# Optimization experiments

Hardware: AMD Instinct MI355X
Metric: run time of the kernel (lower is better)

Reference implementation:

```python
import jax, jax.numpy as jnp
import numpy as np

N_INPUTS = 128
N_LATENT = 21
LEN_TIME = 51
NUM_SHIFTS = 50
BATCH = 2048
N_HIDDEN = 4  # hidden relu layers in the outer DenseResBlock


def setup_inputs() -> dict:
    key = jax.random.key(0)
    ks = jax.random.split(key, 8)
    s = 0.05  # small init scale keeps activations sane through the residual stack
    return {
        "inputs": jax.random.normal(ks[0], (BATCH, LEN_TIME, N_INPUTS), jnp.float32),
        "L": jnp.eye(N_LATENT, dtype=jnp.float32)
             + s * jax.random.normal(ks[1], (N_LATENT, N_LATENT), jnp.float32),
        "ienc_W": s * jax.random.normal(ks[2], (N_INPUTS, N_LATENT), jnp.float32),
        "idec_W": s * jax.random.normal(ks[3], (N_LATENT, N_INPUTS), jnp.float32),
        "enc_W": s * jax.random.normal(ks[4], (N_HIDDEN, N_INPUTS, N_INPUTS), jnp.float32),
        "enc_b": jnp.zeros((N_HIDDEN, N_INPUTS), jnp.float32),
        "enc_Wo": s * jax.random.normal(ks[5], (N_INPUTS, N_INPUTS), jnp.float32),
        "enc_bo": jnp.zeros((N_INPUTS,), jnp.float32),
        "dec_W": s * jax.random.normal(ks[6], (N_HIDDEN, N_INPUTS, N_INPUTS), jnp.float32),
        "dec_b": jnp.zeros((N_HIDDEN, N_INPUTS), jnp.float32),
        "dec_Wo": s * jax.random.normal(ks[7], (N_INPUTS, N_INPUTS), jnp.float32),
        "dec_bo": jnp.zeros((N_INPUTS,), jnp.float32),
    }


def _resblock(x, W, b, Wo, bo):
    # DenseResBlock: stack of relu Dense layers + linear output + residual skip.
    h = x
    for i in range(W.shape[0]):  # fixed small layer count
        h = jax.nn.relu(h @ W[i] + b[i])
    return x + h @ Wo + bo


def reference(inputs, L, ienc_W, idec_W, enc_W, enc_b, enc_Wo, enc_bo,
              dec_W, dec_b, dec_Wo, dec_bo):
    B, T, n_in = inputs.shape
    len_pred = T - NUM_SHIFTS  # = 1

    auto_in = inputs.reshape(-1, n_in)                        # [B*T, n_in]
    pred_in = inputs[:, :len_pred, :].reshape(-1, n_in)       # [B*len_pred, n_in]

    # autoencoder path
    pe = _resblock(auto_in, enc_W, enc_b, enc_Wo, enc_bo)     # partially encoded
    fe = pe @ ienc_W                                          # fully encoded [., n_latent]
    pd = fe @ idec_W                                          # partially decoded
    autoencoder_output = _resblock(pd, dec_W, dec_b, dec_Wo, dec_bo)
    outer_auto_output = _resblock(pe, dec_W, dec_b, dec_Wo, dec_bo)

    # latent rollout: z_{k+1} = z_k @ L, decode every step
    pe_pred = _resblock(pred_in, enc_W, enc_b, enc_Wo, enc_bo)
    z0 = pe_pred @ ienc_W                                     # [B*len_pred, n_latent]

    def step(z, _):
        z_next = z @ L
        return z_next, z_next

    _, zs = jax.lax.scan(step, z0, None, length=NUM_SHIFTS)   # [S, B*len_pred, n_latent]

    # decode all shifts in one large batched pass (same math as per-shift decode)
    dec_in = zs.reshape(-1, zs.shape[-1]) @ idec_W            # [S*B*len_pred, n_in]
    dec_all = _resblock(dec_in, dec_W, dec_b, dec_Wo, dec_bo)
    predictions = (dec_all
                   .reshape(NUM_SHIFTS, B, len_pred, n_in)
                   .transpose(1, 0, 2, 3)
                   .reshape(B, NUM_SHIFTS * len_pred, n_in))

    return autoencoder_output, outer_auto_output, predictions
```

## Files before the change

### kernel.cpp

```cpp
#include <hip/hip_runtime.h>

#define NF 128
#define NLAT 21
#define NBATCH 2048
#define LEN_T 51
#define NSHIFT 50
#define AUTO_ROWS (NBATCH*LEN_T)
#define PRED_ROWS (NBATCH*NSHIFT)

typedef short bh8  __attribute__((ext_vector_type(8)));
typedef unsigned short us8 __attribute__((ext_vector_type(8)));
typedef float f32x4  __attribute__((ext_vector_type(4)));
typedef float f32x16 __attribute__((ext_vector_type(16)));
typedef unsigned u32x4 __attribute__((ext_vector_type(4)));

#define MFMA32(A,B,C) __builtin_amdgcn_mfma_f32_32x32x16_bf16(A,B,C,0,0,0)
#define SGB(m,n) __builtin_amdgcn_sched_group_barrier((m),(n),0)

__device__ __forceinline__ float bf2f(short s){
  unsigned u = ((unsigned)(unsigned short)s) << 16;
  return __builtin_bit_cast(float, u);
}
__device__ __forceinline__ short f2bf(float v){
  unsigned u = __builtin_bit_cast(unsigned, v);
  return (short)((u + 0x7FFFu + ((u>>16)&1u)) >> 16);
}
__device__ __forceinline__ unsigned pk2(float a, float b){
  unsigned ua = __builtin_bit_cast(unsigned, a) + 0x8000u;
  unsigned ub = __builtin_bit_cast(unsigned, b) + 0x8000u;
  return (ua >> 16) | (ub & 0xFFFF0000u);
}

__global__ void k_mmul(const float* __restrict__ ienc, const float* __restrict__ idec,
                       float* __restrict__ M){
  int idx = blockIdx.x*256 + threadIdx.x;
  int i = idx>>7, j = idx&127;
  float s = 0.f;
#pragma unroll
  for(int k=0;k<NLAT;++k) s = fmaf(ienc[i*NLAT+k], idec[k*NF+j], s);
  M[idx] = s;
}

__global__ void k_prep(const float* __restrict__ encW, const float* __restrict__ encWo,
                       const float* __restrict__ decW, const float* __restrict__ decWo,
                       const float* __restrict__ M,    const float* __restrict__ idec,
                       unsigned short* __restrict__ swz){
  int id  = blockIdx.x*256 + threadIdx.x;
  int mat = id >> 11;
  int rem = id & 2047;
  int f   = rem >> 6, l = rem & 63;
  int s   = f >> 2,  mt = f & 3;
  int hl  = l >> 5,  c  = l & 31;
  const float* src;
  if(mat<4)       src = encW + mat*16384;
  else if(mat==4) src = encWo;
  else if(mat<9)  src = decW + (mat-5)*16384;
  else if(mat==9) src = decWo;
  else if(mat==10)src = M;
  else            src = idec;
  us8 w8;
#pragma unroll
  for(int i=0;i<8;++i){
    int k = s*16 + 4*hl + (i&3) + 8*(i>>2);
    float v;
    if(mat==11) v = (k<NLAT) ? src[k*NF + mt*32 + c] : 0.f;
    else        v = src[k*NF + mt*32 + c];
    w8[i] = (unsigned short)f2bf(v);
  }
  *(us8*)(swz + (size_t)mat*16384 + (size_t)f*512 + (size_t)l*8) = w8;
}

__device__ __forceinline__ bh8 ldg8(const unsigned short* p){ return *(const bh8*)p; }

__device__ __forceinline__ void run_half(const unsigned short* __restrict__ wg, int m,
    const bh8 h[16], f32x16 acc[4], int lane){
  f32x16 z;
#pragma unroll
  for(int r=0;r<16;++r) z[r]=0.f;
  acc[0]=z; acc[1]=z; acc[2]=z; acc[3]=z;
  const unsigned short* base = wg + m*1024 + lane*8;
  bh8 w0a = ldg8(base);
  bh8 w0b = ldg8(base + 512);
  bh8 w1a = ldg8(base + 2048);
  bh8 w1b = ldg8(base + 2048 + 512);
#pragma unroll
  for(int s=0;s<8;++s){
    bh8 na, nb;
    if(s<6){
      na = ldg8(base + (s+2)*2048);
      nb = ldg8(base + (s+2)*2048 + 512);
      SGB(0x20,2);
    }
    __builtin_amdgcn_s_setprio(1);
    acc[0]=MFMA32(w0a,h[s],  acc[0]);
    acc[1]=MFMA32(w0b,h[s],  acc[1]);
    acc[2]=MFMA32(w0a,h[8+s],acc[2]);
    acc[3]=MFMA32(w0b,h[8+s],acc[3]);
    __builtin_amdgcn_s_setprio(0);
    SGB(0x8,4);
    if(s<6){ w0a=w1a; w0b=w1b; w1a=na; w1b=nb; }
    else    { w0a=w1a; w0b=w1b; }
  }
}

__device__ __forceinline__ void run_half_k2(const unsigned short* __restrict__ wg, int m,
    const bh8 zf[4], f32x16 acc[4], int lane){
  f32x16 z;
#pragma unroll
  for(int r=0;r<16;++r) z[r]=0.f;
  acc[0]=z; acc[1]=z; acc[2]=z; acc[3]=z;
  const unsigned short* base = wg + m*1024 + lane*8;
#pragma unroll
  for(int s=0;s<2;++s){
    bh8 a0 = ldg8(base + s*2048);
    bh8 a1 = ldg8(base + s*2048 + 512);
    acc[0]=MFMA32(a0,zf[s],  acc[0]);
    acc[1]=MFMA32(a1,zf[s],  acc[1]);
    acc[2]=MFMA32(a0,zf[2+s],acc[2]);
    acc[3]=MFMA32(a1,zf[2+s],acc[3]);
  }
}

__device__ __forceinline__ void epi_hidden_half(const f32x16 acc[4], const float* __restrict__ bl,
    int m, int hl, bh8 out[8]){
#pragma unroll
  for(int t=0;t<2;++t){
    f32x4 b[4];
#pragma unroll
    for(int q=0;q<4;++q) b[q] = *(const f32x4*)(bl + (2*m+t)*32 + q*8 + hl*4);
#pragma unroll
    for(int g=0;g<2;++g){
      f32x16 a = acc[g*2+t];
#pragma unroll
      for(int q=0;q<4;++q)
#pragma unroll
        for(int j=0;j<4;++j) a[q*4+j] = fmaxf(a[q*4+j] + b[q][j], 0.f);
#pragma unroll
      for(int p=0;p<2;++p){
        u32x4 w;
#pragma unroll
        for(int j=0;j<4;++j) w[j] = pk2(a[p*8+2*j], a[p*8+2*j+1]);
        out[g*4+t*2+p] = __builtin_bit_cast(bh8, w);
      }
    }
  }
}
__device__ __forceinline__ void epi_plain_half(const f32x16 acc[4], bh8 out[8]){
#pragma unroll
  for(int t=0;t<2;++t)
#pragma unroll
    for(int g=0;g<2;++g){
      f32x16 a = acc[g*2+t];
#pragma unroll
      for(int p=0;p<2;++p){
        u32x4 w;
#pragma unroll
        for(int j=0;j<4;++j) w[j] = pk2(a[p*8+2*j], a[p*8+2*j+1]);
        out[g*4+t*2+p] = __builtin_bit_cast(bh8, w);
      }
    }
}

__device__ __forceinline__ void final_half(float* outp, size_t ro0, size_t ro1,
    const f32x16 acc[4], const float* __restrict__ bo, const bh8 r8[8], int m, int hl){
#pragma unroll
  for(int t=0;t<2;++t){
    f32x4 b[4];
#pragma unroll
    for(int q=0;q<4;++q) b[q]=*(const f32x4*)(bo + (2*m+t)*32 + q*8 + hl*4);
#pragma unroll
    for(int g=0;g<2;++g){
      f32x16 a = acc[g*2+t];
      bh8 r0 = r8[g*4 + t*2], r1 = r8[g*4 + t*2 + 1];
#pragma unroll
      for(int q=0;q<4;++q)
#pragma unroll
        for(int j=0;j<4;++j){
          int r=q*4+j;
          a[r] += b[q][j] + bf2f((r<8 ? r0 : r1)[r&7]);
        }
      size_t ro = g ? ro1 : ro0;
#pragma unroll
      for(int q=0;q<4;++q){
        f32x4 w; w[0]=a[q*4+0]; w[1]=a[q*4+1]; w[2]=a[q*4+2]; w[3]=a[q*4+3];
        *(f32x4*)(outp + ro + (2*m+t)*32 + q*8 + hl*4) = w;
      }
    }
  }
}

__device__ __forceinline__ void peWo_half(const f32x16 acc[4], const float* __restrict__ bo,
    const bh8 r8[8], int m, int hl, bh8 out[8], float* __restrict__ pe0,
    int bidx0, int bidx1, bool isz0, bool isz1){
#pragma unroll
  for(int t=0;t<2;++t){
    f32x4 b[4];
#pragma unroll
    for(int q=0;q<4;++q) b[q]=*(const f32x4*)(bo + (2*m+t)*32 + q*8 + hl*4);
#pragma unroll
    for(int g=0;g<2;++g){
      f32x16 a = acc[g*2+t];
      bh8 r0 = r8[g*4 + t*2], r1 = r8[g*4 + t*2 + 1];
#pragma unroll
      for(int q=0;q<4;++q)
#pragma unroll
        for(int j=0;j<4;++j){
          int r=q*4+j;
          a[r] += b[q][j] + bf2f((r<8 ? r0 : r1)[r&7]);
        }
      bool isz = g ? isz1 : isz0;
      int bidx = g ? bidx1 : bidx0;
      if(isz){
#pragma unroll
        for(int q=0;q<4;++q){
          f32x4 w; w[0]=a[q*4+0]; w[1]=a[q*4+1]; w[2]=a[q*4+2]; w[3]=a[q*4+3];
          *(f32x4*)(pe0 + (size_t)bidx*NF + (2*m+t)*32 + q*8 + hl*4) = w;
        }
      }
#pragma unroll
      for(int p=0;p<2;++p){
        u32x4 w;
#pragma unroll
        for(int j=0;j<4;++j) w[j]=pk2(a[p*8+2*j], a[p*8+2*j+1]);
        out[g*4+t*2+p]=__builtin_bit_cast(bh8,w);
      }
    }
  }
}

__device__ __forceinline__ void layer_hidden(const unsigned short* __restrict__ wg,
    const float* __restrict__ bl, bh8 h[16], int lane, int hl){
  f32x16 acc[4]; bh8 t0[8], t1[8];
  run_half(wg,0,h,acc,lane);
  epi_hidden_half(acc,bl,0,hl,t0);
  run_half(wg,1,h,acc,lane);
  epi_hidden_half(acc,bl,1,hl,t1);
#pragma unroll
  for(int g=0;g<2;++g)
#pragma unroll
    for(int k=0;k<4;++k){ h[g*8+k]=t0[g*4+k]; h[g*8+4+k]=t1[g*4+k]; }
}

__device__ __forceinline__ void stash16(unsigned short* sp, const bh8 h[16], int lane){
#pragma unroll
  for(int f=0;f<16;++f) *(bh8*)(sp + f*512 + lane*8) = h[f];
}
__device__ __forceinline__ void unstash16(const unsigned short* sp, bh8 r[16], int lane){
#pragma unroll
  for(int f=0;f<16;++f) r[f] = *(const bh8*)(sp + f*512 + lane*8);
}
__device__ __forceinline__ void unstash8(const unsigned short* sp, bh8 r8[8], int m, int lane){
#pragma unroll
  for(int g=0;g<2;++g)
#pragma unroll
    for(int k=0;k<4;++k)
      r8[g*4+k] = *(const bh8*)(sp + (g*8 + 4*m + k)*512 + lane*8);
}

__global__ __launch_bounds__(64,2)
void k_main4(const float* __restrict__ gin, const unsigned short* __restrict__ swz,
             const float* __restrict__ encB, const float* __restrict__ encBo,
             const float* __restrict__ decB, const float* __restrict__ decBo,
             float* __restrict__ out1, float* __restrict__ out2, float* __restrict__ pe0){
  __shared__ __align__(16) unsigned short sres[8192];
  const int lane = threadIdx.x;
  const int hl = lane>>5, c31 = lane&31;
  const size_t rowbase = (size_t)blockIdx.x*64;
  const int row0 = (int)rowbase + c31, row1 = row0 + 32;
  const size_t ro0 = (size_t)row0*NF, ro1 = (size_t)row1*NF;
  const int bidx0 = row0/LEN_T, bidx1 = row1/LEN_T;
  const bool isz0 = (row0 == bidx0*LEN_T), isz1 = (row1 == bidx1*LEN_T);
  bh8 h[16];

#pragma unroll
  for(int g=0;g<2;++g){
    const float* rp = gin + (g?ro1:ro0);
#pragma unroll
    for(int s=0;s<8;++s){
      f32x4 a=*(const f32x4*)(rp + s*16 + 4*hl);
      f32x4 b=*(const f32x4*)(rp + s*16 + 8 + 4*hl);
      us8 o;
#pragma unroll
      for(int i=0;i<4;++i){ o[i]=(unsigned short)f2bf(a[i]); o[i+4]=(unsigned short)f2bf(b[i]); }
      h[g*8+s]=__builtin_bit_cast(bh8,o);
    }
  }
  stash16(sres, h, lane);

#pragma unroll 1
  for(int l=0;l<4;++l)
    layer_hidden(swz + (size_t)l*16384, encB + l*NF, h, lane, hl);

  {
    const unsigned short* wg = swz + (size_t)4*16384;
    f32x16 acc[4]; bh8 t0[8], t1[8], r8[8];
    run_half(wg,0,h,acc,lane);
    unstash8(sres, r8, 0, lane);
    peWo_half(acc, encBo, r8, 0, hl, t0, pe0, bidx0,bidx1, isz0,isz1);
    run_half(wg,1,h,acc,lane);
    unstash8(sres, r8, 1, lane);
    peWo_half(acc, encBo, r8, 1, hl, t1, pe0, bidx0,bidx1, isz0,isz1);
#pragma unroll
    for(int g=0;g<2;++g)
#pragma unroll
      for(int k=0;k<4;++k){ h[g*8+k]=t0[g*4+k]; h[g*8+4+k]=t1[g*4+k]; }
    stash16(sres, h, lane);
  }

#pragma unroll 1
  for(int l=0;l<4;++l)
    layer_hidden(swz + (size_t)(5+l)*16384, decB + l*NF, h, lane, hl);

  {
    const unsigned short* wg = swz + (size_t)9*16384;
    f32x16 acc[4]; bh8 r8[8];
    run_half(wg,0,h,acc,lane);
    unstash8(sres, r8, 0, lane);
    final_half(out2, ro0, ro1, acc, decBo, r8, 0, hl);
    run_half(wg,1,h,acc,lane);
    unstash8(sres, r8, 1, lane);
    final_half(out2, ro0, ro1, acc, decBo, r8, 1, hl);
  }

  {
    unstash16(sres, h, lane);
    const unsigned short* wg = swz + (size_t)10*16384;
    f32x16 acc[4]; bh8 t0[8], t1[8];
    run_half(wg,0,h,acc,lane); epi_plain_half(acc,t0);
    run_half(wg,1,h,acc,lane); epi_plain_half(acc,t1);
#pragma unroll
    for(int g=0;g<2;++g)
#pragma unroll
      for(int k=0;k<4;++k){ h[g*8+k]=t0[g*4+k]; h[g*8+4+k]=t1[g*4+k]; }
    stash16(sres, h, lane);
  }

#pragma unroll 1
  for(int l=0;l<4;++l)
    layer_hidden(swz + (size_t)(5+l)*16384, decB + l*NF, h, lane, hl);

  {
    const unsigned short* wg = swz + (size_t)9*16384;
    f32x16 acc[4]; bh8 r8[8];
    run_half(wg,0,h,acc,lane);
    unstash8(sres, r8, 0, lane);
    final_half(out1, ro0, ro1, acc, decBo, r8, 0, hl);
    run_half(wg,1,h,acc,lane);
    unstash8(sres, r8, 1, lane);
    final_half(out1, ro0, ro1, acc, decBo, r8, 1, hl);
  }
}

__global__ void k_roll(const float* __restrict__ pe0, const float* __restrict__ ienc,
                       const float* __restrict__ L, float* __restrict__ zs){
  const int tid=threadIdx.x, lane=tid&63, wid=tid>>6, sub=lane&31, half=lane>>5;
  const int row=blockIdx.x*8 + wid*2 + half;
  const bool act = sub < NLAT;
  float Lc[NLAT];
#pragma unroll
  for(int k=0;k<NLAT;++k) Lc[k] = act ? L[k*NLAT+sub] : 0.f;
  float z=0.f;
  if(act){
    const float* pr = pe0 + (size_t)row*NF;
    float s0=0.f,s1=0.f,s2=0.f,s3=0.f;
#pragma unroll 8
    for(int k=0;k<NF;k+=4){
      s0=fmaf(pr[k+0], ienc[(k+0)*NLAT+sub], s0);
      s1=fmaf(pr[k+1], ienc[(k+1)*NLAT+sub], s1);
      s2=fmaf(pr[k+2], ienc[(k+2)*NLAT+sub], s2);
      s3=fmaf(pr[k+3], ienc[(k+3)*NLAT+sub], s3);
    }
    z=(s0+s1)+(s2+s3);
  }
  const int base = half*32;
#pragma unroll 1
  for(int s=0;s<NSHIFT;++s){
    float zn=0.f;
#pragma unroll
    for(int k=0;k<NLAT;++k) zn=fmaf(__shfl(z, base+k, 64), Lc[k], zn);
    z=zn;
    if(act) zs[((size_t)s*NBATCH + row)*NLAT + sub] = z;
  }
}

__global__ __launch_bounds__(64,2)
void k_pred4(const float* __restrict__ zs, const unsigned short* __restrict__ swz,
             const float* __restrict__ decB, const float* __restrict__ decBo,
             float* __restrict__ out3){
  __shared__ __align__(16) unsigned short sres[8192];
  const int lane = threadIdx.x;
  const int hl = lane>>5, c31 = lane&31;
  const size_t rowbase = (size_t)blockIdx.x*64;
  const int prow0 = (int)rowbase + c31, prow1 = prow0 + 32;
  const int orow0 = (prow0 & 2047)*NSHIFT + (prow0 >> 11);
  const int orow1 = (prow1 & 2047)*NSHIFT + (prow1 >> 11);
  bh8 h[16];

  bh8 zf[4];
#pragma unroll
  for(int g=0;g<2;++g){
    const float* zr = zs + (size_t)(g?prow1:prow0)*NLAT;
#pragma unroll
    for(int s=0;s<2;++s){
      us8 o;
#pragma unroll
      for(int i=0;i<8;++i){
        int cc = s*16 + 4*hl + (i&3) + 8*(i>>2);
        o[i] = (cc<NLAT) ? (unsigned short)f2bf(zr[cc]) : (unsigned short)0;
      }
      zf[g*2+s]=__builtin_bit_cast(bh8,o);
    }
  }

  {
    const unsigned short* wg = swz + (size_t)11*16384;
    f32x16 acc[4]; bh8 t0[8], t1[8];
    run_half_k2(wg,0,zf,acc,lane); epi_plain_half(acc,t0);
    run_half_k2(wg,1,zf,acc,lane); epi_plain_half(acc,t1);
#pragma unroll
    for(int g=0;g<2;++g)
#pragma unroll
      for(int k=0;k<4;++k){ h[g*8+k]=t0[g*4+k]; h[g*8+4+k]=t1[g*4+k]; }
    stash16(sres, h, lane);
  }

#pragma unroll 1
  for(int l=0;l<4;++l)
    layer_hidden(swz + (size_t)(5+l)*16384, decB + l*NF, h, lane, hl);

  {
    const unsigned short* wg = swz + (size_t)9*16384;
    f32x16 acc[4]; bh8 r8[8];
    run_half(wg,0,h,acc,lane);
    unstash8(sres, r8, 0, lane);
    final_half(out3, (size_t)orow0*NF, (size_t)orow1*NF, acc, decBo, r8, 0, hl);
    run_half(wg,1,h,acc,lane);
    unstash8(sres, r8, 1, lane);
    final_half(out3, (size_t)orow0*NF, (size_t)orow1*NF, acc, decBo, r8, 1, hl);
  }
}

extern "C" void kernel_launch(void* const* d_in, const int* in_sizes, int n_in,
                              void* d_out, int out_size, void* d_ws, size_t ws_size,
                              hipStream_t stream) {
  const float* gin   = (const float*)d_in[0];
  const float* L     = (const float*)d_in[1];
  const float* iencW = (const float*)d_in[2];
  const float* idecW = (const float*)d_in[3];
  const float* encW  = (const float*)d_in[4];
  const float* encB  = (const float*)d_in[5];
  const float* encWo = (const float*)d_in[6];
  const float* encBo = (const float*)d_in[7];
  const float* decW  = (const float*)d_in[8];
  const float* decB  = (const float*)d_in[9];
  const float* decWo = (const float*)d_in[10];
  const float* decBo = (const float*)d_in[11];

  float* out1 = (float*)d_out;
  float* out2 = out1 + (size_t)AUTO_ROWS*NF;
  float* out3 = out2 + (size_t)AUTO_ROWS*NF;

  float* M   = (float*)d_ws;
  float* pe0 = M + 16384;
  float* zs  = pe0 + (size_t)NBATCH*NF;
  unsigned short* swz = (unsigned short*)(zs + (size_t)NSHIFT*NBATCH*NLAT);

  hipLaunchKernelGGL(k_mmul, dim3(64),  dim3(256), 0, stream, iencW, idecW, M);
  hipLaunchKernelGGL(k_prep, dim3(96),  dim3(256), 0, stream, encW, encWo, decW, decWo, M, idecW, swz);
  hipLaunchKernelGGL(k_main4, dim3(AUTO_ROWS/64), dim3(64), 0, stream,
                     gin, swz, encB, encBo, decB, decBo, out1, out2, pe0);
  hipLaunchKernelGGL(k_roll, dim3(NBATCH/8), dim3(256), 0, stream, pe0, iencW, L, zs);
  hipLaunchKernelGGL(k_pred4, dim3(PRED_ROWS/64), dim3(64), 0, stream,
                     zs, swz, decB, decBo, out3);
}
```

Measured before the change: 153.2 us.

## Halve rows per wave to cut registers and raise occupancy

Each 64-lane block now processes 32 rows instead of 64. Accumulators, activation fragments and the shared-memory residual stash are halved, and launch bounds rise from 2 to 3 waves per SIMD. Grids for the main and prediction kernels double to match. The aim is more waves in flight to hide weight-load and MFMA latency. The cost is that each weight fragment loaded from global memory or cache feeds half as many MFMAs, so weight traffic per row doubles.

```diff
diff --git a/kernel.cpp b/kernel.cpp
--- a/kernel.cpp
+++ b/kernel.cpp
@@ -73,11 +73,11 @@
 __device__ __forceinline__ bh8 ldg8(const unsigned short* p){ return *(const bh8*)p; }
 
 __device__ __forceinline__ void run_half(const unsigned short* __restrict__ wg, int m,
-    const bh8 h[16], f32x16 acc[4], int lane){
+    const bh8 h[8], f32x16 acc[2], int lane){
   f32x16 z;
 #pragma unroll
   for(int r=0;r<16;++r) z[r]=0.f;
-  acc[0]=z; acc[1]=z; acc[2]=z; acc[3]=z;
+  acc[0]=z; acc[1]=z;
   const unsigned short* base = wg + m*1024 + lane*8;
   bh8 w0a = ldg8(base);
   bh8 w0b = ldg8(base + 512);
@@ -92,189 +92,164 @@
       SGB(0x20,2);
     }
     __builtin_amdgcn_s_setprio(1);
-    acc[0]=MFMA32(w0a,h[s],  acc[0]);
-    acc[1]=MFMA32(w0b,h[s],  acc[1]);
-    acc[2]=MFMA32(w0a,h[8+s],acc[2]);
-    acc[3]=MFMA32(w0b,h[8+s],acc[3]);
+    acc[0]=MFMA32(w0a,h[s],acc[0]);
+    acc[1]=MFMA32(w0b,h[s],acc[1]);
     __builtin_amdgcn_s_setprio(0);
-    SGB(0x8,4);
+    SGB(0x8,2);
     if(s<6){ w0a=w1a; w0b=w1b; w1a=na; w1b=nb; }
     else    { w0a=w1a; w0b=w1b; }
   }
 }
 
 __device__ __forceinline__ void run_half_k2(const unsigned short* __restrict__ wg, int m,
-    const bh8 zf[4], f32x16 acc[4], int lane){
+    const bh8 zf[2], f32x16 acc[2], int lane){
   f32x16 z;
 #pragma unroll
   for(int r=0;r<16;++r) z[r]=0.f;
-  acc[0]=z; acc[1]=z; acc[2]=z; acc[3]=z;
+  acc[0]=z; acc[1]=z;
   const unsigned short* base = wg + m*1024 + lane*8;
 #pragma unroll
   for(int s=0;s<2;++s){
     bh8 a0 = ldg8(base + s*2048);
     bh8 a1 = ldg8(base + s*2048 + 512);
-    acc[0]=MFMA32(a0,zf[s],  acc[0]);
-    acc[1]=MFMA32(a1,zf[s],  acc[1]);
-    acc[2]=MFMA32(a0,zf[2+s],acc[2]);
-    acc[3]=MFMA32(a1,zf[2+s],acc[3]);
-  }
-}
-
-__device__ __forceinline__ void epi_hidden_half(const f32x16 acc[4], const float* __restrict__ bl,
-    int m, int hl, bh8 out[8]){
+    acc[0]=MFMA32(a0,zf[s],acc[0]);
+    acc[1]=MFMA32(a1,zf[s],acc[1]);
+  }
+}
+
+__device__ __forceinline__ void epi_hidden_half(const f32x16 acc[2], const float* __restrict__ bl,
+    int m, int hl, bh8 out[4]){
 #pragma unroll
   for(int t=0;t<2;++t){
     f32x4 b[4];
 #pragma unroll
     for(int q=0;q<4;++q) b[q] = *(const f32x4*)(bl + (2*m+t)*32 + q*8 + hl*4);
-#pragma unroll
-    for(int g=0;g<2;++g){
-      f32x16 a = acc[g*2+t];
-#pragma unroll
-      for(int q=0;q<4;++q)
-#pragma unroll
-        for(int j=0;j<4;++j) a[q*4+j] = fmaxf(a[q*4+j] + b[q][j], 0.f);
-#pragma unroll
-      for(int p=0;p<2;++p){
-        u32x4 w;
-#pragma unroll
-        for(int j=0;j<4;++j) w[j] = pk2(a[p*8+2*j], a[p*8+2*j+1]);
-        out[g*4+t*2+p] = __builtin_bit_cast(bh8, w);
-      }
-    }
-  }
-}
-__device__ __forceinline__ void epi_plain_half(const f32x16 acc[4], bh8 out[8]){
-#pragma unroll
-  for(int t=0;t<2;++t)
-#pragma unroll
-    for(int g=0;g<2;++g){
-      f32x16 a = acc[g*2+t];
-#pragma unroll
-      for(int p=0;p<2;++p){
-        u32x4 w;
-#pragma unroll
-        for(int j=0;j<4;++j) w[j] = pk2(a[p*8+2*j], a[p*8+2*j+1]);
-        out[g*4+t*2+p] = __builtin_bit_cast(bh8, w);
-      }
-    }
-}
-
-__device__ __forceinline__ void final_half(float* outp, size_t ro0, size_t ro1,
-    const f32x16 acc[4], const float* __restrict__ bo, const bh8 r8[8], int m, int hl){
+    f32x16 a = acc[t];
+#pragma unroll
+    for(int q=0;q<4;++q)
+#pragma unroll
+      for(int j=0;j<4;++j) a[q*4+j] = fmaxf(a[q*4+j] + b[q][j], 0.f);
+#pragma unroll
+    for(int p=0;p<2;++p){
+      u32x4 w;
+#pragma unroll
+      for(int j=0;j<4;++j) w[j] = pk2(a[p*8+2*j], a[p*8+2*j+1]);
+      out[t*2+p] = __builtin_bit_cast(bh8, w);
+    }
+  }
+}
+__device__ __forceinline__ void epi_plain_half(const f32x16 acc[2], bh8 out[4]){
+#pragma unroll
+  for(int t=0;t<2;++t){
+    f32x16 a = acc[t];
+#pragma unroll
+    for(int p=0;p<2;++p){
+      u32x4 w;
+#pragma unroll
+      for(int j=0;j<4;++j) w[j] = pk2(a[p*8+2*j], a[p*8+2*j+1]);
+      out[t*2+p] = __builtin_bit_cast(bh8, w);
+    }
+  }
+}
+
+__device__ __forceinline__ void final_half(float* outp, size_t ro,
+    const f32x16 acc[2], const float* __restrict__ bo, const bh8 r4[4], int m, int hl){
 #pragma unroll
   for(int t=0;t<2;++t){
     f32x4 b[4];
 #pragma unroll
     for(int q=0;q<4;++q) b[q]=*(const f32x4*)(bo + (2*m+t)*32 + q*8 + hl*4);
-#pragma unroll
-    for(int g=0;g<2;++g){
-      f32x16 a = acc[g*2+t];
-      bh8 r0 = r8[g*4 + t*2], r1 = r8[g*4 + t*2 + 1];
-#pragma unroll
-      for(int q=0;q<4;++q)
-#pragma unroll
-        for(int j=0;j<4;++j){
-          int r=q*4+j;
-          a[r] += b[q][j] + bf2f((r<8 ? r0 : r1)[r&7]);
-        }
-      size_t ro = g ? ro1 : ro0;
+    f32x16 a = acc[t];
+    bh8 r0 = r4[t*2], r1 = r4[t*2+1];
+#pragma unroll
+    for(int q=0;q<4;++q)
+#pragma unroll
+      for(int j=0;j<4;++j){
+        int r=q*4+j;
+        a[r] += b[q][j] + bf2f((r<8 ? r0 : r1)[r&7]);
+      }
+#pragma unroll
+    for(int q=0;q<4;++q){
+      f32x4 w; w[0]=a[q*4+0]; w[1]=a[q*4+1]; w[2]=a[q*4+2]; w[3]=a[q*4+3];
+      *(f32x4*)(outp + ro + (2*m+t)*32 + q*8 + hl*4) = w;
+    }
+  }
+}
+
+__device__ __forceinline__ void peWo_half(const f32x16 acc[2], const float* __restrict__ bo,
+    const bh8 r4[4], int m, int hl, bh8 out[4], float* __restrict__ pe0,
+    int bidx, bool isz){
+#pragma unroll
+  for(int t=0;t<2;++t){
+    f32x4 b[4];
+#pragma unroll
+    for(int q=0;q<4;++q) b[q]=*(const f32x4*)(bo + (2*m+t)*32 + q*8 + hl*4);
+    f32x16 a = acc[t];
+    bh8 r0 = r4[t*2], r1 = r4[t*2+1];
+#pragma unroll
+    for(int q=0;q<4;++q)
+#pragma unroll
+      for(int j=0;j<4;++j){
+        int r=q*4+j;
+        a[r] += b[q][j] + bf2f((r<8 ? r0 : r1)[r&7]);
+      }
+    if(isz){
 #pragma unroll
       for(int q=0;q<4;++q){
         f32x4 w; w[0]=a[q*4+0]; w[1]=a[q*4+1]; w[2]=a[q*4+2]; w[3]=a[q*4+3];
-        *(f32x4*)(outp + ro + (2*m+t)*32 + q*8 + hl*4) = w;
+        *(f32x4*)(pe0 + (size_t)bidx*NF + (2*m+t)*32 + q*8 + hl*4) = w;
       }
     }
-  }
-}
-
-__device__ __forceinline__ void peWo_half(const f32x16 acc[4], const float* __restrict__ bo,
-    const bh8 r8[8], int m, int hl, bh8 out[8], float* __restrict__ pe0,
-    int bidx0, int bidx1, bool isz0, bool isz1){
-#pragma unroll
-  for(int t=0;t<2;++t){
-    f32x4 b[4];
-#pragma unroll
-    for(int q=0;q<4;++q) b[q]=*(const f32x4*)(bo + (2*m+t)*32 + q*8 + hl*4);
-#pragma unroll
-    for(int g=0;g<2;++g){
-      f32x16 a = acc[g*2+t];
-      bh8 r0 = r8[g*4 + t*2], r1 = r8[g*4 + t*2 + 1];
-#pragma unroll
-      for(int q=0;q<4;++q)
-#pragma unroll
-        for(int j=0;j<4;++j){
-          int r=q*4+j;
-          a[r] += b[q][j] + bf2f((r<8 ? r0 : r1)[r&7]);
-        }
-      bool isz = g ? isz1 : isz0;
-      int bidx = g ? bidx1 : bidx0;
-      if(isz){
-#pragma unroll
-        for(int q=0;q<4;++q){
-          f32x4 w; w[0]=a[q*4+0]; w[1]=a[q*4+1]; w[2]=a[q*4+2]; w[3]=a[q*4+3];
-          *(f32x4*)(pe0 + (size_t)bidx*NF + (2*m+t)*32 + q*8 + hl*4) = w;
-        }
-      }
-#pragma unroll
-      for(int p=0;p<2;++p){
-        u32x4 w;
-#pragma unroll
-        for(int j=0;j<4;++j) w[j]=pk2(a[p*8+2*j], a[p*8+2*j+1]);
-        out[g*4+t*2+p]=__builtin_bit_cast(bh8,w);
-      }
+#pragma unroll
+    for(int p=0;p<2;++p){
+      u32x4 w;
+#pragma unroll
+      for(int j=0;j<4;++j) w[j]=pk2(a[p*8+2*j], a[p*8+2*j+1]);
+      out[t*2+p]=__builtin_bit_cast(bh8,w);
     }
   }
 }
 
 __device__ __forceinline__ void layer_hidden(const unsigned short* __restrict__ wg,
-    const float* __restrict__ bl, bh8 h[16], int lane, int hl){
-  f32x16 acc[4]; bh8 t0[8], t1[8];
+    const float* __restrict__ bl, bh8 h[8], int lane, int hl){
+  f32x16 acc[2]; bh8 t0[4], t1[4];
   run_half(wg,0,h,acc,lane);
   epi_hidden_half(acc,bl,0,hl,t0);
   run_half(wg,1,h,acc,lane);
   epi_hidden_half(acc,bl,1,hl,t1);
 #pragma unroll
-  for(int g=0;g<2;++g)
-#pragma unroll
-    for(int k=0;k<4;++k){ h[g*8+k]=t0[g*4+k]; h[g*8+4+k]=t1[g*4+k]; }
-}
-
-__device__ __forceinline__ void stash16(unsigned short* sp, const bh8 h[16], int lane){
-#pragma unroll
-  for(int f=0;f<16;++f) *(bh8*)(sp + f*512 + lane*8) = h[f];
-}
-__device__ __forceinline__ void unstash16(const unsigned short* sp, bh8 r[16], int lane){
-#pragma unroll
-  for(int f=0;f<16;++f) r[f] = *(const bh8*)(sp + f*512 + lane*8);
-}
-__device__ __forceinline__ void unstash8(const unsigned short* sp, bh8 r8[8], int m, int lane){
-#pragma unroll
-  for(int g=0;g<2;++g)
-#pragma unroll
-    for(int k=0;k<4;++k)
-      r8[g*4+k] = *(const bh8*)(sp + (g*8 + 4*m + k)*512 + lane*8);
-}
-
-__global__ __launch_bounds__(64,2)
-void k_main4(const float* __restrict__ gin, const unsigned short* __restrict__ swz,
+  for(int k=0;k<4;++k){ h[k]=t0[k]; h[4+k]=t1[k]; }
+}
+
+__device__ __forceinline__ void stash8(unsigned short* sp, const bh8 h[8], int lane){
+#pragma unroll
+  for(int f=0;f<8;++f) *(bh8*)(sp + f*512 + lane*8) = h[f];
+}
+__device__ __forceinline__ void unstash8f(const unsigned short* sp, bh8 r[8], int lane){
+#pragma unroll
+  for(int f=0;f<8;++f) r[f] = *(const bh8*)(sp + f*512 + lane*8);
+}
+__device__ __forceinline__ void unstash4(const unsigned short* sp, bh8 r4[4], int m, int lane){
+#pragma unroll
+  for(int k=0;k<4;++k) r4[k] = *(const bh8*)(sp + (4*m+k)*512 + lane*8);
+}
+
+__global__ __launch_bounds__(64,3)
+void k_main5(const float* __restrict__ gin, const unsigned short* __restrict__ swz,
              const float* __restrict__ encB, const float* __restrict__ encBo,
              const float* __restrict__ decB, const float* __restrict__ decBo,
              float* __restrict__ out1, float* __restrict__ out2, float* __restrict__ pe0){
-  __shared__ __align__(16) unsigned short sres[8192];
+  __shared__ __align__(16) unsigned short sres[4096];
   const int lane = threadIdx.x;
   const int hl = lane>>5, c31 = lane&31;
-  const size_t rowbase = (size_t)blockIdx.x*64;
-  const int row0 = (int)rowbase + c31, row1 = row0 + 32;
-  const size_t ro0 = (size_t)row0*NF, ro1 = (size_t)row1*NF;
-  const int bidx0 = row0/LEN_T, bidx1 = row1/LEN_T;
-  const bool isz0 = (row0 == bidx0*LEN_T), isz1 = (row1 == bidx1*LEN_T);
-  bh8 h[16];
-
-#pragma unroll
-  for(int g=0;g<2;++g){
-    const float* rp = gin + (g?ro1:ro0);
+  const int row = blockIdx.x*32 + c31;
+  const size_t ro = (size_t)row*NF;
+  const int bidx = row/LEN_T;
+  const bool isz = (row == bidx*LEN_T);
+  bh8 h[8];
+
+  {
+    const float* rp = gin + ro;
 #pragma unroll
     for(int s=0;s<8;++s){
       f32x4 a=*(const f32x4*)(rp + s*16 + 4*hl);
@@ -282,10 +257,10 @@
       us8 o;
 #pragma unroll
       for(int i=0;i<4;++i){ o[i]=(unsigned short)f2bf(a[i]); o[i+4]=(unsigned short)f2bf(b[i]); }
-      h[g*8+s]=__builtin_bit_cast(bh8,o);
-    }
-  }
-  stash16(sres, h, lane);
+      h[s]=__builtin_bit_cast(bh8,o);
+    }
+  }
+  stash8(sres, h, lane);
 
 #pragma unroll 1
   for(int l=0;l<4;++l)
@@ -293,18 +268,16 @@
 
   {
     const unsigned short* wg = swz + (size_t)4*16384;
-    f32x16 acc[4]; bh8 t0[8], t1[8], r8[8];
+    f32x16 acc[2]; bh8 t0[4], t1[4], r4[4];
     run_half(wg,0,h,acc,lane);
-    unstash8(sres, r8, 0, lane);
-    peWo_half(acc, encBo, r8, 0, hl, t0, pe0, bidx0,bidx1, isz0,isz1);
+    unstash4(sres, r4, 0, lane);
+    peWo_half(acc, encBo, r4, 0, hl, t0, pe0, bidx, isz);
     run_half(wg,1,h,acc,lane);
-    unstash8(sres, r8, 1, lane);
-    peWo_half(acc, encBo, r8, 1, hl, t1, pe0, bidx0,bidx1, isz0,isz1);
-#pragma unroll
-    for(int g=0;g<2;++g)
-#pragma unroll
-      for(int k=0;k<4;++k){ h[g*8+k]=t0[g*4+k]; h[g*8+4+k]=t1[g*4+k]; }
-    stash16(sres, h, lane);
+    unstash4(sres, r4, 1, lane);
+    peWo_half(acc, encBo, r4, 1, hl, t1, pe0, bidx, isz);
+#pragma unroll
+    for(int k=0;k<4;++k){ h[k]=t0[k]; h[4+k]=t1[k]; }
+    stash8(sres, h, lane);
   }
 
 #pragma unroll 1
@@ -313,26 +286,24 @@
 
   {
     const unsigned short* wg = swz + (size_t)9*16384;
-    f32x16 acc[4]; bh8 r8[8];
+    f32x16 acc[2]; bh8 r4[4];
     run_half(wg,0,h,acc,lane);
-    unstash8(sres, r8, 0, lane);
-    final_half(out2, ro0, ro1, acc, decBo, r8, 0, hl);
+    unstash4(sres, r4, 0, lane);
+    final_half(out2, ro, acc, decBo, r4, 0, hl);
     run_half(wg,1,h,acc,lane);
-    unstash8(sres, r8, 1, lane);
-    final_half(out2, ro0, ro1, acc, decBo, r8, 1, hl);
-  }
-
-  {
-    unstash16(sres, h, lane);
+    unstash4(sres, r4, 1, lane);
+    final_half(out2, ro, acc, decBo, r4, 1, hl);
+  }
+
+  {
+    unstash8f(sres, h, lane);
     const unsigned short* wg = swz + (size_t)10*16384;
-    f32x16 acc[4]; bh8 t0[8], t1[8];
+    f32x16 acc[2]; bh8 t0[4], t1[4];
     run_half(wg,0,h,acc,lane); epi_plain_half(acc,t0);
     run_half(wg,1,h,acc,lane); epi_plain_half(acc,t1);
 #pragma unroll
-    for(int g=0;g<2;++g)
-#pragma unroll
-      for(int k=0;k<4;++k){ h[g*8+k]=t0[g*4+k]; h[g*8+4+k]=t1[g*4+k]; }
-    stash16(sres, h, lane);
+    for(int k=0;k<4;++k){ h[k]=t0[k]; h[4+k]=t1[k]; }
+    stash8(sres, h, lane);
   }
 
 #pragma unroll 1
@@ -341,13 +312,13 @@
 
   {
     const unsigned short* wg = swz + (size_t)9*16384;
-    f32x16 acc[4]; bh8 r8[8];
+    f32x16 acc[2]; bh8 r4[4];
     run_half(wg,0,h,acc,lane);
-    unstash8(sres, r8, 0, lane);
-    final_half(out1, ro0, ro1, acc, decBo, r8, 0, hl);
+    unstash4(sres, r4, 0, lane);
+    final_half(out1, ro, acc, decBo, r4, 0, hl);
     run_half(wg,1,h,acc,lane);
-    unstash8(sres, r8, 1, lane);
-    final_half(out1, ro0, ro1, acc, decBo, r8, 1, hl);
+    unstash4(sres, r4, 1, lane);
+    final_half(out1, ro, acc, decBo, r4, 1, hl);
   }
 }
 
@@ -383,23 +354,21 @@
   }
 }
 
-__global__ __launch_bounds__(64,2)
-void k_pred4(const float* __restrict__ zs, const unsigned short* __restrict__ swz,
+__global__ __launch_bounds__(64,3)
+void k_pred5(const float* __restrict__ zs, const unsigned short* __restrict__ swz,
              const float* __restrict__ decB, const float* __restrict__ decBo,
              float* __restrict__ out3){
-  __shared__ __align__(16) unsigned short sres[8192];
+  __shared__ __align__(16) unsigned short sres[4096];
   const int lane = threadIdx.x;
   const int hl = lane>>5, c31 = lane&31;
-  const size_t rowbase = (size_t)blockIdx.x*64;
-  const int prow0 = (int)rowbase + c31, prow1 = prow0 + 32;
-  const int orow0 = (prow0 & 2047)*NSHIFT + (prow0 >> 11);
-  const int orow1 = (prow1 & 2047)*NSHIFT + (prow1 >> 11);
-  bh8 h[16];
-
-  bh8 zf[4];
-#pragma unroll
-  for(int g=0;g<2;++g){
-    const float* zr = zs + (size_t)(g?prow1:prow0)*NLAT;
+  const int prow = blockIdx.x*32 + c31;
+  const int orow = (prow & 2047)*NSHIFT + (prow >> 11);
+  const size_t oro = (size_t)orow*NF;
+  bh8 h[8];
+
+  bh8 zf[2];
+  {
+    const float* zr = zs + (size_t)prow*NLAT;
 #pragma unroll
     for(int s=0;s<2;++s){
       us8 o;
@@ -408,20 +377,18 @@
         int cc = s*16 + 4*hl + (i&3) + 8*(i>>2);
         o[i] = (cc<NLAT) ? (unsigned short)f2bf(zr[cc]) : (unsigned short)0;
       }
-      zf[g*2+s]=__builtin_bit_cast(bh8,o);
+      zf[s]=__builtin_bit_cast(bh8,o);
     }
   }
 
   {
     const unsigned short* wg = swz + (size_t)11*16384;
-    f32x16 acc[4]; bh8 t0[8], t1[8];
+    f32x16 acc[2]; bh8 t0[4], t1[4];
     run_half_k2(wg,0,zf,acc,lane); epi_plain_half(acc,t0);
     run_half_k2(wg,1,zf,acc,lane); epi_plain_half(acc,t1);
 #pragma unroll
-    for(int g=0;g<2;++g)
-#pragma unroll
-      for(int k=0;k<4;++k){ h[g*8+k]=t0[g*4+k]; h[g*8+4+k]=t1[g*4+k]; }
-    stash16(sres, h, lane);
+    for(int k=0;k<4;++k){ h[k]=t0[k]; h[4+k]=t1[k]; }
+    stash8(sres, h, lane);
   }
 
 #pragma unroll 1
@@ -430,13 +397,13 @@
 
   {
     const unsigned short* wg = swz + (size_t)9*16384;
-    f32x16 acc[4]; bh8 r8[8];
+    f32x16 acc[2]; bh8 r4[4];
     run_half(wg,0,h,acc,lane);
-    unstash8(sres, r8, 0, lane);
-    final_half(out3, (size_t)orow0*NF, (size_t)orow1*NF, acc, decBo, r8, 0, hl);
+    unstash4(sres, r4, 0, lane);
+    final_half(out3, oro, acc, decBo, r4, 0, hl);
     run_half(wg,1,h,acc,lane);
-    unstash8(sres, r8, 1, lane);
-    final_half(out3, (size_t)orow0*NF, (size_t)orow1*NF, acc, decBo, r8, 1, hl);
+    unstash4(sres, r4, 1, lane);
+    final_half(out3, oro, acc, decBo, r4, 1, hl);
   }
 }
 
@@ -467,9 +434,9 @@
 
   hipLaunchKernelGGL(k_mmul, dim3(64),  dim3(256), 0, stream, iencW, idecW, M);
   hipLaunchKernelGGL(k_prep, dim3(96),  dim3(256), 0, stream, encW, encWo, decW, decWo, M, idecW, swz);
-  hipLaunchKernelGGL(k_main4, dim3(AUTO_ROWS/64), dim3(64), 0, stream,
+  hipLaunchKernelGGL(k_main5, dim3(AUTO_ROWS/32), dim3(64), 0, stream,
                      gin, swz, encB, encBo, decB, decBo, out1, out2, pe0);
   hipLaunchKernelGGL(k_roll, dim3(NBATCH/8), dim3(256), 0, stream, pe0, iencW, L, zs);
-  hipLaunchKernelGGL(k_pred4, dim3(PRED_ROWS/64), dim3(64), 0, stream,
+  hipLaunchKernelGGL(k_pred5, dim3(PRED_ROWS/32), dim3(64), 0, stream,
                      zs, swz, decB, decBo, out3);
 }
```

Result: slower. 190.7 us (+24.4%).
